# Performance work log

Measured on AMD Instinct MI355X. Metric: run time of the kernel, lower is better.

The kernel has to match this reference:

```python
import math
import jax, jax.numpy as jnp
import numpy as np

H = 2048
T = 8192
NUM_LAYERS = 24
LAYER_ID = 6


def setup_inputs() -> dict:
    key = jax.random.key(0)
    ks = jax.random.split(key, 5)
    ratio_0_to_1 = LAYER_ID / (NUM_LAYERS - 1)
    ratio_1_to_almost_0 = 1.0 - LAYER_ID / NUM_LAYERS
    # parameter init exactly as in RwkvSelfAttention.__init__
    zigzag = 0.5 * (jnp.arange(1, H + 1) % 3 - 1)
    time_first = jnp.full((H,), math.log(0.3), jnp.float32) + zigzag.astype(jnp.float32)
    hh = jnp.arange(0, H, dtype=jnp.float32)
    time_decay = -5.0 + 8.0 * (hh / (H - 1)) ** (0.7 + 1.3 * ratio_0_to_1)
    xx = jnp.arange(H, dtype=jnp.float32) / H
    time_mix_key = jnp.power(xx, ratio_1_to_almost_0)
    time_mix_value = time_mix_key + 0.3 * ratio_0_to_1
    time_mix_receptance = jnp.power(xx, 0.5 * ratio_1_to_almost_0)
    scale = 1.0 / math.sqrt(H)
    return {
        "hidden": jax.random.normal(ks[0], (T, H), jnp.float32),
        "sx": jnp.zeros((H,), jnp.float32),
        "aa": jnp.zeros((H,), jnp.float32),
        "bb": jnp.zeros((H,), jnp.float32),
        "pp": jnp.full((H,), -1e30, jnp.float32),  # log-space -inf init
        "time_decay": time_decay,
        "time_first": time_first,
        "time_mix_key": time_mix_key,
        "time_mix_value": time_mix_value,
        "time_mix_receptance": time_mix_receptance,
        "Wk": jax.random.normal(ks[1], (H, H), jnp.float32) * scale,
        "Wv": jax.random.normal(ks[2], (H, H), jnp.float32) * scale,
        "Wr": jax.random.normal(ks[3], (H, H), jnp.float32) * scale,
        "Wo": jax.random.normal(ks[4], (H, H), jnp.float32) * scale,
    }


def reference(hidden, sx, aa, bb, pp, time_decay, time_first, time_mix_key,
              time_mix_value, time_mix_receptance, Wk, Wv, Wr, Wo):
    # token-shift mix: c_x[t] = hidden[t-1], c_x[0] = sx
    c_x = jnp.concatenate((sx[None, :], hidden[:-1, :]), axis=0)  # [T, H]
    key_x = hidden * time_mix_key + c_x * (1.0 - time_mix_key)
    value_x = hidden * time_mix_value + c_x * (1.0 - time_mix_value)
    receptance_x = hidden * time_mix_receptance + c_x * (1.0 - time_mix_receptance)

    r = jax.nn.sigmoid(receptance_x @ Wr)  # [T, H]
    k = key_x @ Wk                         # [T, H]
    v = value_x @ Wv                       # [T, H]

    w_decay = -jnp.exp(time_decay)  # [H]

    def step(state, kv):
        a, b, p = state
        kk, vv = kv
        # output with bonus (time_first)
        ww = time_first + kk
        q = jnp.maximum(p, ww)
        e1 = jnp.exp(p - q)
        e2 = jnp.exp(ww - q)
        out_t = (e1 * a + e2 * vv) / (e1 * b + e2)
        # state update with decay
        ww2 = w_decay + p
        q2 = jnp.maximum(ww2, kk)
        e1b = jnp.exp(ww2 - q2)
        e2b = jnp.exp(kk - q2)
        return (e1b * a + e2b * vv, e1b * b + e2b, q2), out_t

    (aa, bb, pp), wkv = jax.lax.scan(step, (aa, bb, pp), (k, v))  # wkv: [T, H]

    out = hidden + (r * wkv) @ Wo
    return out, hidden[-1, :], aa, bb, pp
```

## Files before the change

### kernel.cpp

```cpp
#include <hip/hip_runtime.h>
#include <stdint.h>

#define H 2048
#define T 8192
#define C_CH 128
#define L_CH 64

typedef unsigned short u16;
typedef unsigned int u32;

__device__ __forceinline__ float bf2f(u16 u) {
  return __uint_as_float(((u32)u) << 16);
}
__device__ __forceinline__ u16 f2bf(float f) {
  u32 u = __float_as_uint(f);
  u = u + 0x7FFFu + ((u >> 16) & 1u);
  return (u16)(u >> 16);
}
__device__ __forceinline__ bool in_is_bf16(const u32* ppw) {
  u32 w = ppw[0];
  return (w >> 16) == (w & 0xFFFFu);
}
__device__ __forceinline__ float ldin(const void* p, size_t i, bool bf) {
  return bf ? bf2f(((const u16*)p)[i]) : ((const float*)p)[i];
}
__device__ __forceinline__ void stout(void* p, size_t i, float v, bool bf) {
  if (bf) ((u16*)p)[i] = f2bf(v);
  else ((float*)p)[i] = v;
}

__global__ void mix3_kernel(const void* __restrict__ hidden,
                            const void* __restrict__ sx,
                            const void* __restrict__ tmk,
                            const void* __restrict__ tmv,
                            const void* __restrict__ tmr,
                            u16* __restrict__ outk, u16* __restrict__ outv,
                            u16* __restrict__ outr, const u32* __restrict__ ppw) {
  bool bf = in_is_bf16(ppw);
  int i = blockIdx.x * blockDim.x + threadIdx.x;
  int h = i & (H - 1);
  float hv = ldin(hidden, (size_t)i, bf);
  float cv = (i < H) ? ldin(sx, (size_t)h, bf) : ldin(hidden, (size_t)i - H, bf);
  float d = hv - cv;
  outk[i] = f2bf(cv + ldin(tmk, (size_t)h, bf) * d);
  outv[i] = f2bf(cv + ldin(tmv, (size_t)h, bf) * d);
  outr[i] = f2bf(cv + ldin(tmr, (size_t)h, bf) * d);
}

__global__ void transpose_kernel(const void* __restrict__ W, u16* __restrict__ Wt,
                                 const u32* __restrict__ ppw) {
  bool bf = in_is_bf16(ppw);
  __shared__ u16 tile[32][33];
  int bx = blockIdx.x * 32, by = blockIdx.y * 32;
  int tx = threadIdx.x, ty = threadIdx.y;
#pragma unroll
  for (int j = 0; j < 32; j += 8)
    tile[ty + j][tx] = f2bf(ldin(W, (size_t)(by + ty + j) * H + bx + tx, bf));
  __syncthreads();
#pragma unroll
  for (int j = 0; j < 32; j += 8)
    Wt[(size_t)(bx + ty + j) * H + by + tx] = tile[tx][ty + j];
}

typedef short bf16x8 __attribute__((ext_vector_type(8)));
typedef float f32x4 __attribute__((ext_vector_type(4)));
typedef float f32x2 __attribute__((ext_vector_type(2)));

#define MODE_K 0
#define MODE_BF16 1
#define MODE_SIG 2
#define MODE_ADDH 3

__device__ __forceinline__ void gl_lds16(const short* g, short* l) {
  __builtin_amdgcn_global_load_lds((__attribute__((address_space(1))) void*)(g),
                                   (__attribute__((address_space(3))) void*)(l),
                                   16, 0, 0);
}

template <int MODE>
__global__ __launch_bounds__(512, 4) void gemm_kernel(
    const u16* __restrict__ Au, const u16* __restrict__ Btu,
    void* __restrict__ C, const void* __restrict__ hid,
    const u32* __restrict__ ppw) {
  __shared__ alignas(16) char lds_raw[73728];
  short* const As0 = (short*)lds_raw;
  short* const Bs0 = (short*)lds_raw + 3 * 8192;
  const short* A = (const short*)Au;
  const short* Bt = (const short*)Btu;

  const int bid = blockIdx.x;
  const int xcd = bid & 7;
  const int s = bid >> 3;
  const int mblk = (xcd << 2) | (s & 3);
  const int nblk = s >> 2;
  const int m0 = mblk * 256;
  const int n0 = nblk * 128;

  const int tid = threadIdx.x;
  const int lane = tid & 63;
  const int wid = tid >> 6;
  const int wm = wid >> 1;
  const int wn = wid & 1;
  const int lrow = lane & 15;
  const int quad = lane >> 4;

  const int srow = lane >> 2;
  const int schunk = (lane & 3) ^ ((lane >> 3) & 3);
  const short* gA = A + (size_t)(m0 + wid * 32 + srow) * H + schunk * 8;
  const short* gB = Bt + (size_t)(n0 + wid * 16 + srow) * H + schunk * 8;

  const int gxor = (quad ^ ((lrow >> 1) & 3)) * 8;
  const int arow = (wm * 64 + lrow) * 32 + gxor;
  const int brow = (wn * 64 + lrow) * 32 + gxor;

  f32x4 acc[4][4];
#pragma unroll
  for (int i = 0; i < 4; i++)
#pragma unroll
    for (int j = 0; j < 4; j++) acc[i][j] = (f32x4){0.f, 0.f, 0.f, 0.f};

  const int NT = H / 32;

#define STAGE_TILE(koff, sl)                                   \
  do {                                                         \
    short* la = As0 + (sl)*8192 + wid * 1024;                  \
    short* lb = Bs0 + (sl)*4096 + wid * 512;                   \
    gl_lds16(gA + (koff), la);                                 \
    gl_lds16(gA + (koff) + (size_t)16 * H, la + 512);          \
    gl_lds16(gB + (koff), lb);                                 \
  } while (0)

  STAGE_TILE(0, 0);
  STAGE_TILE(32, 1);
  asm volatile("s_waitcnt vmcnt(3)" ::: "memory");
  __builtin_amdgcn_sched_barrier(0);
  __builtin_amdgcn_s_barrier();

  for (int tau = 0; tau < NT; ++tau) {
    const int rd = tau % 3;
    const int st = (tau + 2) % 3;
    const short* asl = As0 + rd * 8192;
    const short* bsl = Bs0 + rd * 4096;

    bf16x8 af[4], bfv[4];
#pragma unroll
    for (int i = 0; i < 4; i++)
      af[i] = *(const bf16x8*)(asl + arow + i * 512);
#pragma unroll
    for (int j = 0; j < 4; j++)
      bfv[j] = *(const bf16x8*)(bsl + brow + j * 512);

    if (tau <= NT - 3) STAGE_TILE((size_t)(tau + 2) * 32, st);

    __builtin_amdgcn_s_setprio(1);
#pragma unroll
    for (int i = 0; i < 4; i++)
#pragma unroll
      for (int j = 0; j < 4; j++)
        acc[i][j] = __builtin_amdgcn_mfma_f32_16x16x32_bf16(af[i], bfv[j],
                                                            acc[i][j], 0, 0, 0);
    __builtin_amdgcn_s_setprio(0);

    if (tau <= NT - 3) {
      asm volatile("s_waitcnt vmcnt(3)" ::: "memory");
    } else if (tau == NT - 2) {
      asm volatile("s_waitcnt vmcnt(0)" ::: "memory");
    }
    __builtin_amdgcn_sched_barrier(0);
    if (tau < NT - 1) __builtin_amdgcn_s_barrier();
  }
#undef STAGE_TILE

  __builtin_amdgcn_s_barrier();
  {
    bool bf = (MODE == MODE_ADDH) ? in_is_bf16(ppw) : true;
    float* lC = (float*)lds_raw + (size_t)wid * (32 * 66);
    const int el = lane & 31;
    const int eh = lane >> 5;
#pragma unroll
    for (int p = 0; p < 2; p++) {
#pragma unroll
      for (int ih = 0; ih < 2; ih++) {
        const int i = p * 2 + ih;
#pragma unroll
        for (int j = 0; j < 4; j++)
#pragma unroll
          for (int reg = 0; reg < 4; reg++)
            lC[(ih * 16 + quad * 4 + reg) * 66 + j * 16 + lrow] =
                acc[i][j][reg];
      }
#pragma unroll
      for (int k = 0; k < 16; k++) {
        const int rr = k * 2 + eh;
        f32x2 v = *(const f32x2*)(lC + rr * 66 + el * 2);
        const int row = m0 + wm * 64 + p * 32 + rr;
        const int col = n0 + wn * 64 + el * 2;
        size_t idx = (size_t)row * H + col;
        if (MODE == MODE_SIG) {
          v[0] = 1.0f / (1.0f + __expf(-v[0]));
          v[1] = 1.0f / (1.0f + __expf(-v[1]));
        }
        if (MODE == MODE_ADDH) {
          if (bf) {
            u32 hv = *(const u32*)((const u16*)hid + idx);
            v[0] += bf2f((u16)(hv & 0xFFFFu));
            v[1] += bf2f((u16)(hv >> 16));
            u32 pk = (u32)f2bf(v[0]) | ((u32)f2bf(v[1]) << 16);
            *(u32*)((u16*)C + idx) = pk;
          } else {
            f32x2 hv = *(const f32x2*)((const float*)hid + idx);
            v[0] += hv[0];
            v[1] += hv[1];
            *(f32x2*)((float*)C + idx) = v;
          }
        } else {
          u32 pk = (u32)f2bf(v[0]) | ((u32)f2bf(v[1]) << 16);
          *(u32*)((u16*)C + idx) = pk;
        }
      }
    }
  }
}

__global__ __launch_bounds__(256) void wkv_local_kernel(
    const u16* __restrict__ kbuf, const u16* __restrict__ vbuf,
    const void* __restrict__ tdec,
    float* __restrict__ suma, float* __restrict__ sumb, float* __restrict__ sump,
    const u32* __restrict__ ppw) {
  bool bf = in_is_bf16(ppw);
  int h = blockIdx.x * 256 + threadIdx.x;
  int c = blockIdx.y;
  float w = -__expf(ldin(tdec, h, bf));
  float a = 0.f, b = 0.f, p = -1e30f;
  size_t base = (size_t)c * L_CH * H + h;
#pragma unroll 4
  for (int t = 0; t < L_CH; t++) {
    size_t idx = base + (size_t)t * H;
    float kk = bf2f(kbuf[idx]);
    float vv = bf2f(vbuf[idx]);
    float ww2 = w + p;
    float q2 = fmaxf(ww2, kk);
    float e1b = __expf(ww2 - q2), e2b = __expf(kk - q2);
    a = e1b * a + e2b * vv;
    b = e1b * b + e2b;
    p = q2;
  }
  suma[(size_t)c * H + h] = a;
  sumb[(size_t)c * H + h] = b;
  sump[(size_t)c * H + h] = p;
}

__global__ __launch_bounds__(256) void wkv_prefix_kernel(
    const float* __restrict__ suma, const float* __restrict__ sumb,
    const float* __restrict__ sump,
    const void* __restrict__ aa_in, const void* __restrict__ bb_in,
    const void* __restrict__ pp_in, const void* __restrict__ tdec,
    const void* __restrict__ hidden,
    float* __restrict__ sta, float* __restrict__ stb, float* __restrict__ stp,
    void* __restrict__ dout, const u32* __restrict__ ppw) {
  bool bf = in_is_bf16(ppw);
  int h = blockIdx.x * 256 + threadIdx.x;
  float a = ldin(aa_in, h, bf), b = ldin(bb_in, h, bf), p = ldin(pp_in, h, bf);
  float w = -__expf(ldin(tdec, h, bf));
  float wL = w * (float)L_CH;
  for (int c = 0; c < C_CH; c++) {
    size_t i = (size_t)c * H + h;
    sta[i] = a;
    stb[i] = b;
    stp[i] = p;
    float la = suma[i], lb = sumb[i], lp = sump[i];
    float pd = p + wL;
    float q = fmaxf(pd, lp);
    float e1 = __expf(pd - q), e2 = __expf(lp - q);
    a = e1 * a + e2 * la;
    b = e1 * b + e2 * lb;
    p = q;
  }
  size_t base = (size_t)T * H;
  stout(dout, base + h, ldin(hidden, (size_t)(T - 1) * H + h, bf), bf);
  stout(dout, base + H + h, a, bf);
  stout(dout, base + 2 * H + h, b, bf);
  stout(dout, base + 3 * H + h, p, bf);
}

__global__ __launch_bounds__(256) void wkv_out_kernel(
    const u16* __restrict__ kbuf, const u16* __restrict__ vbuf,
    const u16* __restrict__ rbuf,
    const float* __restrict__ sta, const float* __restrict__ stb,
    const float* __restrict__ stp,
    const void* __restrict__ tdec, const void* __restrict__ tfirst,
    u16* __restrict__ rw, const u32* __restrict__ ppw) {
  bool bf = in_is_bf16(ppw);
  int h = blockIdx.x * 256 + threadIdx.x;
  int c = blockIdx.y;
  size_t si = (size_t)c * H + h;
  float a = sta[si], b = stb[si], p = stp[si];
  float tf = ldin(tfirst, h, bf);
  float w = -__expf(ldin(tdec, h, bf));
  size_t base = (size_t)c * L_CH * H + h;
#pragma unroll 4
  for (int t = 0; t < L_CH; t++) {
    size_t idx = base + (size_t)t * H;
    float kk = bf2f(kbuf[idx]);
    float vv = bf2f(vbuf[idx]);
    float rr = bf2f(rbuf[idx]);
    float ww = tf + kk;
    float q = fmaxf(p, ww);
    float e1 = __expf(p - q), e2 = __expf(ww - q);
    float wkv = (e1 * a + e2 * vv) / (e1 * b + e2);
    rw[idx] = f2bf(rr * wkv);
    float ww2 = w + p;
    float q2 = fmaxf(ww2, kk);
    float e1b = __expf(ww2 - q2), e2b = __expf(kk - q2);
    a = e1b * a + e2b * vv;
    b = e1b * b + e2b;
    p = q2;
  }
}

extern "C" void kernel_launch(void* const* d_in, const int* in_sizes, int n_in,
                              void* d_out, int out_size, void* d_ws, size_t ws_size,
                              hipStream_t stream) {
  const void* hidden = d_in[0];
  const void* sx = d_in[1];
  const void* aa = d_in[2];
  const void* bb = d_in[3];
  const void* pp = d_in[4];
  const void* tdec = d_in[5];
  const void* tfirst = d_in[6];
  const void* tmk = d_in[7];
  const void* tmv = d_in[8];
  const void* tmr = d_in[9];
  const void* Wk = d_in[10];
  const void* Wv = d_in[11];
  const void* Wr = d_in[12];
  const void* Wo = d_in[13];
  const u32* ppw = (const u32*)d_in[4];

  char* ws = (char*)d_ws;
  const size_t TH2 = (size_t)T * H * 2;
  const size_t WT2 = (size_t)H * H * 2;
  u16* A1 = (u16*)ws;
  u16* A2 = (u16*)(ws + TH2);
  u16* A3 = (u16*)(ws + 2 * TH2);
  u16* B1 = (u16*)(ws + 3 * TH2);
  u16* Wt_buf = (u16*)(ws + 4 * TH2);
  float* suma = (float*)(ws + 4 * TH2 + WT2);
  float* sumb = suma + (size_t)C_CH * H;
  float* sump = sumb + (size_t)C_CH * H;
  float* sta = sump + (size_t)C_CH * H;
  float* stb = sta + (size_t)C_CH * H;
  float* stp = stb + (size_t)C_CH * H;

  dim3 mixG((T * H) / 256), mixB(256);
  dim3 trG(64, 64), trB(32, 8);
  dim3 gG(512), gB(512);
  dim3 scG(H / 256, C_CH), scB(256);

  mix3_kernel<<<mixG, mixB, 0, stream>>>(hidden, sx, tmk, tmv, tmr,
                                         A1, A2, A3, ppw);
  transpose_kernel<<<trG, trB, 0, stream>>>(Wr, Wt_buf, ppw);
  gemm_kernel<MODE_SIG><<<gG, gB, 0, stream>>>(A3, Wt_buf, B1, nullptr, ppw);
  transpose_kernel<<<trG, trB, 0, stream>>>(Wk, Wt_buf, ppw);
  gemm_kernel<MODE_K><<<gG, gB, 0, stream>>>(A1, Wt_buf, A3, nullptr, ppw);
  transpose_kernel<<<trG, trB, 0, stream>>>(Wv, Wt_buf, ppw);
  gemm_kernel<MODE_BF16><<<gG, gB, 0, stream>>>(A2, Wt_buf, A1, nullptr, ppw);
  wkv_local_kernel<<<scG, scB, 0, stream>>>(A3, A1, tdec, suma, sumb, sump, ppw);
  wkv_prefix_kernel<<<dim3(H / 256), scB, 0, stream>>>(
      suma, sumb, sump, aa, bb, pp, tdec, hidden, sta, stb, stp, d_out, ppw);
  wkv_out_kernel<<<scG, scB, 0, stream>>>(A3, A1, B1, sta, stb, stp,
                                          tdec, tfirst, A2, ppw);
  transpose_kernel<<<trG, trB, 0, stream>>>(Wo, Wt_buf, ppw);
  gemm_kernel<MODE_ADDH><<<gG, gB, 0, stream>>>(A2, Wt_buf, d_out, hidden, ppw);
}
```

Baseline: 597.2 us.

## Load GEMM B operand straight into double-buffered registers, bypassing LDS

The B tile no longer goes through LDS staging. Each wave now loads its B fragments from global memory directly into registers, using a two-phase register double buffer, while A keeps its three-slot LDS pipeline. The goal is to cut LDS footprint, LDS read traffic and staging instructions for B. In exchange, the four wm-waves sharing a column block each load the same B data redundantly from global/L2. The global-load latency also now sits inside each phase's wait, which it may not fully hide.

Measured after the change: 910.6 us. +52.5%, slower.

```diff
diff --git a/kernel.cpp b/kernel.cpp
--- a/kernel.cpp
+++ b/kernel.cpp
@@ -82,9 +82,8 @@
     const u16* __restrict__ Au, const u16* __restrict__ Btu,
     void* __restrict__ C, const void* __restrict__ hid,
     const u32* __restrict__ ppw) {
-  __shared__ alignas(16) char lds_raw[73728];
+  __shared__ alignas(16) char lds_raw[67584];
   short* const As0 = (short*)lds_raw;
-  short* const Bs0 = (short*)lds_raw + 3 * 8192;
   const short* A = (const short*)Au;
   const short* Bt = (const short*)Btu;
 
@@ -107,11 +106,11 @@
   const int srow = lane >> 2;
   const int schunk = (lane & 3) ^ ((lane >> 3) & 3);
   const short* gA = A + (size_t)(m0 + wid * 32 + srow) * H + schunk * 8;
-  const short* gB = Bt + (size_t)(n0 + wid * 16 + srow) * H + schunk * 8;
 
   const int gxor = (quad ^ ((lrow >> 1) & 3)) * 8;
   const int arow = (wm * 64 + lrow) * 32 + gxor;
-  const int brow = (wn * 64 + lrow) * 32 + gxor;
+
+  const short* gBr = Bt + (size_t)(n0 + wn * 64 + lrow) * H + quad * 8;
 
   f32x4 acc[4][4];
 #pragma unroll
@@ -121,55 +120,60 @@
 
   const int NT = H / 32;
 
-#define STAGE_TILE(koff, sl)                                   \
-  do {                                                         \
-    short* la = As0 + (sl)*8192 + wid * 1024;                  \
-    short* lb = Bs0 + (sl)*4096 + wid * 512;                   \
-    gl_lds16(gA + (koff), la);                                 \
-    gl_lds16(gA + (koff) + (size_t)16 * H, la + 512);          \
-    gl_lds16(gB + (koff), lb);                                 \
-  } while (0)
-
-  STAGE_TILE(0, 0);
-  STAGE_TILE(32, 1);
-  asm volatile("s_waitcnt vmcnt(3)" ::: "memory");
+  bf16x8 bA[4], bB[4];
+
+  {
+    gl_lds16(gA, As0 + wid * 1024);
+    gl_lds16(gA + (size_t)16 * H, As0 + wid * 1024 + 512);
+    gl_lds16(gA + 32, As0 + 8192 + wid * 1024);
+    gl_lds16(gA + 32 + (size_t)16 * H, As0 + 8192 + wid * 1024 + 512);
+#pragma unroll
+    for (int j = 0; j < 4; j++)
+      bA[j] = *(const bf16x8*)(gBr + (size_t)j * 16 * H);
+  }
+  asm volatile("s_waitcnt vmcnt(0)" ::: "memory");
   __builtin_amdgcn_sched_barrier(0);
   __builtin_amdgcn_s_barrier();
 
-  for (int tau = 0; tau < NT; ++tau) {
-    const int rd = tau % 3;
-    const int st = (tau + 2) % 3;
-    const short* asl = As0 + rd * 8192;
-    const short* bsl = Bs0 + rd * 4096;
-
-    bf16x8 af[4], bfv[4];
-#pragma unroll
-    for (int i = 0; i < 4; i++)
-      af[i] = *(const bf16x8*)(asl + arow + i * 512);
-#pragma unroll
-    for (int j = 0; j < 4; j++)
-      bfv[j] = *(const bf16x8*)(bsl + brow + j * 512);
-
-    if (tau <= NT - 3) STAGE_TILE((size_t)(tau + 2) * 32, st);
-
-    __builtin_amdgcn_s_setprio(1);
-#pragma unroll
-    for (int i = 0; i < 4; i++)
-#pragma unroll
-      for (int j = 0; j < 4; j++)
-        acc[i][j] = __builtin_amdgcn_mfma_f32_16x16x32_bf16(af[i], bfv[j],
-                                                            acc[i][j], 0, 0, 0);
-    __builtin_amdgcn_s_setprio(0);
-
-    if (tau <= NT - 3) {
-      asm volatile("s_waitcnt vmcnt(3)" ::: "memory");
-    } else if (tau == NT - 2) {
-      asm volatile("s_waitcnt vmcnt(0)" ::: "memory");
-    }
-    __builtin_amdgcn_sched_barrier(0);
-    if (tau < NT - 1) __builtin_amdgcn_s_barrier();
-  }
-#undef STAGE_TILE
+#define PHASE(tau, bu, bl)                                                    \
+  {                                                                           \
+    const int rd = (tau) % 3;                                                 \
+    const int st = ((tau) + 2) % 3;                                           \
+    const short* asl = As0 + rd * 8192;                                       \
+    bf16x8 af[4];                                                             \
+    _Pragma("unroll") for (int i = 0; i < 4; i++)                             \
+        af[i] = *(const bf16x8*)(asl + arow + i * 512);                       \
+    if ((tau) <= NT - 2) {                                                    \
+      _Pragma("unroll") for (int j = 0; j < 4; j++)                           \
+          bl[j] = *(const bf16x8*)(gBr + (size_t)j * 16 * H +                 \
+                                   (size_t)((tau) + 1) * 32);                 \
+    }                                                                         \
+    if ((tau) <= NT - 3) {                                                    \
+      short* la = As0 + st * 8192 + wid * 1024;                               \
+      gl_lds16(gA + (size_t)((tau) + 2) * 32, la);                            \
+      gl_lds16(gA + (size_t)((tau) + 2) * 32 + (size_t)16 * H, la + 512);     \
+    }                                                                         \
+    __builtin_amdgcn_s_setprio(1);                                            \
+    _Pragma("unroll") for (int i = 0; i < 4; i++)                             \
+      _Pragma("unroll") for (int j = 0; j < 4; j++)                           \
+          acc[i][j] = __builtin_amdgcn_mfma_f32_16x16x32_bf16(af[i], bu[j],   \
+                                                              acc[i][j],     \
+                                                              0, 0, 0);       \
+    __builtin_amdgcn_s_setprio(0);                                            \
+    if ((tau) <= NT - 3) {                                                    \
+      asm volatile("s_waitcnt vmcnt(2)" ::: "memory");                        \
+    } else if ((tau) == NT - 2) {                                             \
+      asm volatile("s_waitcnt vmcnt(0)" ::: "memory");                        \
+    }                                                                         \
+    __builtin_amdgcn_sched_barrier(0);                                        \
+    if ((tau) < NT - 1) __builtin_amdgcn_s_barrier();                         \
+  }
+
+  for (int t2 = 0; t2 < NT; t2 += 2) {
+    PHASE(t2, bA, bB);
+    PHASE(t2 + 1, bB, bA);
+  }
+#undef PHASE
 
   __builtin_amdgcn_s_barrier();
   {
```
